# Kernel tuning notes

Measured on AMD Instinct MI355X. Metric: run time of the kernel, lower is better.

## Reference

```python
import jax, jax.numpy as jnp
import numpy as np

B, C = 4096, 10000
TAU = 1.0
MIN_K, MAX_K = 30, 100


def setup_inputs() -> dict:
    key = jax.random.key(0)
    k1, k2 = jax.random.split(key, 2)
    logit = jax.random.normal(k1, (B, C), dtype=jnp.float32)
    target = jax.random.randint(k2, (B,), 0, C)
    # long-tailed class counts: exponential decay from 1000 down to 5
    cls_num = np.exp(np.linspace(np.log(1000.0), np.log(5.0), C)).astype(np.float32)
    cls_num_ratio = cls_num / cls_num.sum()
    log_cls_num = jnp.asarray(np.log(cls_num_ratio + 1e-6), dtype=jnp.float32)
    freq = (cls_num.max() / cls_num).astype(np.float32)
    freq_norm = (freq - freq.min()) / (freq.max() - freq.min() + 1e-6)
    k_per_class = jnp.asarray((freq_norm * (MAX_K - MIN_K) + MIN_K).astype(np.int32))
    return {"logit": logit, "target": target, "log_cls_num": log_cls_num,
            "k_per_class": k_per_class}


def reference(logit, target, log_cls_num, k_per_class):
    b, c = logit.shape
    rows = jnp.arange(b)
    # logit-adjusted cross entropy (loss_full)
    logit_adj = logit + TAU * log_cls_num[None, :]
    log_p_adj = jax.nn.log_softmax(logit_adj, axis=1)  # [B, C]
    loss_full = -jnp.mean(log_p_adj[rows, target])
    # per-row variable-k top-k mask on the ORIGINAL logits
    prob_adj = jnp.exp(log_p_adj)
    k = jnp.minimum(k_per_class[target], c)            # [B]
    sorted_desc = -jnp.sort(-logit, axis=1)            # [B, C] descending
    thresh = sorted_desc[rows, k - 1]                  # k-th largest per row
    mask = logit >= thresh[:, None]
    masked_prob = jnp.where(mask, prob_adj, 0.0) + 1e-6
    masked_prob = masked_prob / masked_prob.sum(axis=1, keepdims=True)
    loss_topk = -jnp.mean(jnp.log(masked_prob)[rows, target])
    return 0.5 * loss_full + 0.5 * loss_topk
```

## Files before the change

kernel.cpp:

```cpp
#include <hip/hip_runtime.h>

#define BLOCK 256
#define C_DIM 10000
#define C4 (C_DIM / 4)
#define NIT ((C4 + BLOCK - 1) / BLOCK)
#define TAU 1.0f
#define CAP 2048
#define PIV_HI 2.0f
#define PIV_LO 1.0f

__device__ __forceinline__ unsigned flip_key(float f) {
    unsigned u = __float_as_uint(f);
    return (u & 0x80000000u) ? ~u : (u | 0x80000000u);
}
__device__ __forceinline__ float unflip_key(unsigned k) {
    unsigned u = (k & 0x80000000u) ? (k & 0x7fffffffu) : ~k;
    return __uint_as_float(u);
}

__global__ void zero_out_kernel(float* out, int n) {
    int i = blockIdx.x * blockDim.x + threadIdx.x;
    if (i < n) out[i] = 0.f;
}

__device__ __forceinline__ void scan_pick(unsigned* hist, int shift, int tid,
                                          unsigned* shp, unsigned* shkr, unsigned* shcnt) {
    unsigned h0 = hist[4 * tid + 0], h1 = hist[4 * tid + 1];
    unsigned h2 = hist[4 * tid + 2], h3 = hist[4 * tid + 3];
    unsigned loc = h0 + h1 + h2 + h3;
    unsigned suf = loc;
    for (int off = 1; off < 64; off <<= 1) {
        unsigned o = __shfl_down(suf, off);
        if (tid + off < 64) suf += o;
    }
    unsigned sufex = suf - loc;
    unsigned kr = *shkr;
    unsigned s3 = sufex + h3;
    unsigned s2 = s3 + h2;
    unsigned s1 = s2 + h1;
    unsigned s0 = s1 + h0;
    int bsel = -1; unsigned newkr = 0, newcnt = 0;
    if      (s3 >= kr && s3 - h3 < kr) { bsel = 4 * tid + 3; newkr = kr - (s3 - h3); newcnt = h3; }
    else if (s2 >= kr && s2 - h2 < kr) { bsel = 4 * tid + 2; newkr = kr - (s2 - h2); newcnt = h2; }
    else if (s1 >= kr && s1 - h1 < kr) { bsel = 4 * tid + 1; newkr = kr - (s1 - h1); newcnt = h1; }
    else if (s0 >= kr && s0 - h0 < kr) { bsel = 4 * tid + 0; newkr = kr - (s0 - h0); newcnt = h0; }
    if (bsel >= 0) {
        *shp |= ((unsigned)bsel << shift);
        *shkr = newkr;
        *shcnt = newcnt;
    }
}

__global__ __launch_bounds__(BLOCK, 8) void topk_la_loss_kernel(
    const float* __restrict__ logit, const int* __restrict__ target,
    const float* __restrict__ lcn, const int* __restrict__ kpc,
    float* __restrict__ out, int B) {
    __shared__ unsigned hist[256];
    __shared__ unsigned candk[CAP];
    __shared__ unsigned short candi[CAP];
    __shared__ float red_a[4], red_b[4];
    __shared__ unsigned sh_nc, sh_prefix, sh_kr, sh_cnt;
    __shared__ int sh_path, sh_k;
    __shared__ float sh_thresh, sh_madj;

    const int row = blockIdx.x;
    const int tid = threadIdx.x;
    const int lane = tid & 63;
    const int wid = tid >> 6;
    const float* lrow = logit + (size_t)row * C_DIM;

    if (tid == 0) {
        int t = target[row];
        int k = kpc[t];
        if (k > C_DIM) k = C_DIM;
        sh_k = k;
        sh_nc = 0u;
    }
    __syncthreads();

    float z = 0.f, madj = -INFINITY;
    for (int it = 0; it < NIT; ++it) {
        int j4 = it * BLOCK + tid;
        if (j4 < C4) {
            float4 f = ((const float4*)lrow)[j4];
            float4 l = ((const float4*)lcn)[j4];
            float a0 = f.x + TAU * l.x, a1 = f.y + TAU * l.y;
            float a2 = f.z + TAU * l.z, a3 = f.w + TAU * l.w;
            z += __expf(a0) + __expf(a1) + __expf(a2) + __expf(a3);
            madj = fmaxf(madj, fmaxf(fmaxf(a0, a1), fmaxf(a2, a3)));
            int j = 4 * j4;
            if (f.x >= PIV_HI) { unsigned i = atomicAdd(&sh_nc, 1u); if (i < CAP) { candk[i] = __float_as_uint(f.x); candi[i] = (unsigned short)(j + 0); } }
            if (f.y >= PIV_HI) { unsigned i = atomicAdd(&sh_nc, 1u); if (i < CAP) { candk[i] = __float_as_uint(f.y); candi[i] = (unsigned short)(j + 1); } }
            if (f.z >= PIV_HI) { unsigned i = atomicAdd(&sh_nc, 1u); if (i < CAP) { candk[i] = __float_as_uint(f.z); candi[i] = (unsigned short)(j + 2); } }
            if (f.w >= PIV_HI) { unsigned i = atomicAdd(&sh_nc, 1u); if (i < CAP) { candk[i] = __float_as_uint(f.w); candi[i] = (unsigned short)(j + 3); } }
        }
    }
    for (int off = 32; off; off >>= 1) madj = fmaxf(madj, __shfl_down(madj, off));
    if (lane == 0) red_a[wid] = madj;
    __syncthreads();

    if (tid == 0) {
        sh_madj = fmaxf(fmaxf(red_a[0], red_a[1]), fmaxf(red_a[2], red_a[3]));
        unsigned n = sh_nc;
        unsigned k = (unsigned)sh_k;
        sh_path = (n >= k && n <= CAP) ? 0 : ((n < k) ? 1 : 2);
        sh_kr = k;
        sh_prefix = 0u;
        sh_cnt = n;
    }
    __syncthreads();

    if (sh_path == 1) {
        if (tid == 0) sh_nc = 0u;
        __syncthreads();
        for (int it = 0; it < NIT; ++it) {
            int j4 = it * BLOCK + tid;
            if (j4 < C4) {
                float4 f = ((const float4*)lrow)[j4];
                int j = 4 * j4;
                if (f.x >= PIV_LO) { unsigned i = atomicAdd(&sh_nc, 1u); if (i < CAP) { candk[i] = __float_as_uint(f.x); candi[i] = (unsigned short)(j + 0); } }
                if (f.y >= PIV_LO) { unsigned i = atomicAdd(&sh_nc, 1u); if (i < CAP) { candk[i] = __float_as_uint(f.y); candi[i] = (unsigned short)(j + 1); } }
                if (f.z >= PIV_LO) { unsigned i = atomicAdd(&sh_nc, 1u); if (i < CAP) { candk[i] = __float_as_uint(f.z); candi[i] = (unsigned short)(j + 2); } }
                if (f.w >= PIV_LO) { unsigned i = atomicAdd(&sh_nc, 1u); if (i < CAP) { candk[i] = __float_as_uint(f.w); candi[i] = (unsigned short)(j + 3); } }
            }
        }
        __syncthreads();
        if (tid == 0) {
            unsigned n = sh_nc;
            unsigned k = (unsigned)sh_k;
            sh_path = (n >= k && n <= CAP) ? 0 : 2;
            sh_kr = k;
            sh_prefix = 0u;
            sh_cnt = n;
        }
        __syncthreads();
    }

    const int path = sh_path;
    const float madjB = sh_madj;

    if (path == 0) {
        const int nc = (int)sh_cnt;
        unsigned kmask = 0u;
        for (int q = 0; q < 4; ++q) {
            if (sh_cnt == 1u) break;
            const int shift = 24 - 8 * q;
            hist[tid] = 0u;
            __syncthreads();
            const unsigned pref = sh_prefix;
            for (int i = tid; i < nc; i += BLOCK) {
                unsigned kk = candk[i];
                if ((kk & kmask) == pref) atomicAdd(&hist[(kk >> shift) & 0xFFu], 1u);
            }
            __syncthreads();
            if (tid < 64) scan_pick(hist, shift, tid, &sh_prefix, &sh_kr, &sh_cnt);
            kmask |= (0xFFu << shift);
            __syncthreads();
        }
        if (sh_cnt == 1u && kmask != 0xFFFFFFFFu) {
            const unsigned pref = sh_prefix;
            __syncthreads();
            for (int i = tid; i < nc; i += BLOCK) {
                unsigned kk = candk[i];
                if ((kk & kmask) == pref) sh_prefix = kk;
            }
            __syncthreads();
        }
        if (tid == 0) sh_thresh = __uint_as_float(sh_prefix);
    } else {
        for (int p = 0; p < 4; ++p) {
            const int shift = 24 - 8 * p;
            const unsigned pmask = p ? (0xFFFFFFFFu << (shift + 8)) : 0u;
            hist[tid] = 0u;
            __syncthreads();
            const unsigned pref = sh_prefix;
            for (int it = 0; it < NIT; ++it) {
                int j4 = it * BLOCK + tid;
                if (j4 < C4) {
                    float4 f = ((const float4*)lrow)[j4];
                    unsigned kk;
                    kk = flip_key(f.x); if ((kk & pmask) == pref) atomicAdd(&hist[(kk >> shift) & 0xFFu], 1u);
                    kk = flip_key(f.y); if ((kk & pmask) == pref) atomicAdd(&hist[(kk >> shift) & 0xFFu], 1u);
                    kk = flip_key(f.z); if ((kk & pmask) == pref) atomicAdd(&hist[(kk >> shift) & 0xFFu], 1u);
                    kk = flip_key(f.w); if ((kk & pmask) == pref) atomicAdd(&hist[(kk >> shift) & 0xFFu], 1u);
                }
            }
            __syncthreads();
            if (tid < 64) scan_pick(hist, shift, tid, &sh_prefix, &sh_kr, &sh_cnt);
            __syncthreads();
        }
        if (tid == 0) sh_thresh = unflip_key(sh_prefix);
    }
    __syncthreads();

    const float thresh = sh_thresh;
    const bool rare = fabsf(madjB) > 80.f;

    float sm = 0.f;
    if (!rare) {
        if (path == 0) {
            const int nc = (int)((sh_nc <= CAP) ? sh_nc : CAP);
            for (int i = tid; i < nc; i += BLOCK) {
                unsigned kk = candk[i];
                float v = __uint_as_float(kk);
                if (v >= thresh) sm += __expf(v + TAU * lcn[candi[i]]);
            }
        } else {
            for (int it = 0; it < NIT; ++it) {
                int j4 = it * BLOCK + tid;
                if (j4 < C4) {
                    float4 f = ((const float4*)lrow)[j4];
                    float4 l = ((const float4*)lcn)[j4];
                    if (f.x >= thresh) sm += __expf(f.x + TAU * l.x);
                    if (f.y >= thresh) sm += __expf(f.y + TAU * l.y);
                    if (f.z >= thresh) sm += __expf(f.z + TAU * l.z);
                    if (f.w >= thresh) sm += __expf(f.w + TAU * l.w);
                }
            }
        }
    } else {
        z = 0.f;
        for (int it = 0; it < NIT; ++it) {
            int j4 = it * BLOCK + tid;
            if (j4 < C4) {
                float4 f = ((const float4*)lrow)[j4];
                float4 l = ((const float4*)lcn)[j4];
                float e;
                e = __expf(f.x + TAU * l.x - madjB); z += e; if (f.x >= thresh) sm += e;
                e = __expf(f.y + TAU * l.y - madjB); z += e; if (f.y >= thresh) sm += e;
                e = __expf(f.z + TAU * l.z - madjB); z += e; if (f.z >= thresh) sm += e;
                e = __expf(f.w + TAU * l.w - madjB); z += e; if (f.w >= thresh) sm += e;
            }
        }
    }

    for (int off = 32; off; off >>= 1) {
        z  += __shfl_down(z, off);
        sm += __shfl_down(sm, off);
    }
    if (lane == 0) { red_a[wid] = z; red_b[wid] = sm; }
    __syncthreads();

    if (tid == 0) {
        float Z = red_a[0] + red_a[1] + red_a[2] + red_a[3];
        float S = red_b[0] + red_b[1] + red_b[2] + red_b[3];
        int t = target[row];
        float logit_t = lrow[t];
        float adj_t = logit_t + TAU * lcn[t];
        float sub = rare ? madjB : 0.f;
        float lpt = adj_t - sub - __logf(Z);
        float p_num = ((logit_t >= thresh) ? __expf(lpt) : 0.f) + 1e-6f;
        float Smask = S / Z + (float)C_DIM * 1e-6f;
        float loss = 0.5f * (-lpt + __logf(Smask) - __logf(p_num));
        atomicAdd(out, loss / (float)B);
    }
}

extern "C" void kernel_launch(void* const* d_in, const int* in_sizes, int n_in,
                              void* d_out, int out_size, void* d_ws, size_t ws_size,
                              hipStream_t stream) {
    const float* logit  = (const float*)d_in[0];
    const int*   target = (const int*)d_in[1];
    const float* lcn    = (const float*)d_in[2];
    const int*   kpc    = (const int*)d_in[3];
    float* out = (float*)d_out;
    const int B = in_sizes[1];

    zero_out_kernel<<<1, 64, 0, stream>>>(out, out_size);
    topk_la_loss_kernel<<<B, BLOCK, 0, stream>>>(logit, target, lcn, kpc, out, B);
}
```

Baseline: 268.0 us.

## Split row pass into segmented streaming kernel and candidate-based select kernel

```diff
diff --git a/kernel.cpp b/kernel.cpp
--- a/kernel.cpp
+++ b/kernel.cpp
@@ -5,9 +5,11 @@
 #define C4 (C_DIM / 4)
 #define NIT ((C4 + BLOCK - 1) / BLOCK)
 #define TAU 1.0f
-#define CAP 2048
-#define PIV_HI 2.0f
-#define PIV_LO 1.0f
+#define PIV 2.0f
+#define SEG 4
+#define SEGLEN (C_DIM / SEG)
+#define SEGLEN4 (SEGLEN / 4)
+#define MAXCAP 2048
 
 __device__ __forceinline__ unsigned flip_key(float f) {
     unsigned u = __float_as_uint(f);
@@ -18,9 +20,73 @@
     return __uint_as_float(u);
 }
 
-__global__ void zero_out_kernel(float* out, int n) {
+__global__ void init_kernel(float* out, int out_n, float* z, unsigned* madj,
+                            unsigned* cnt, int B) {
     int i = blockIdx.x * blockDim.x + threadIdx.x;
-    if (i < n) out[i] = 0.f;
+    if (i < out_n) out[i] = 0.f;
+    if (i < B) { z[i] = 0.f; madj[i] = 0u; cnt[i] = 0u; }
+}
+
+__device__ __forceinline__ void append_cand(bool m, float v, int idx, int lane,
+                                            unsigned* g_cnt_row,
+                                            float* __restrict__ cv,
+                                            unsigned short* __restrict__ ci, int cap) {
+    unsigned long long mk = __ballot(m);
+    if (mk == 0ull) return;
+    int leader = (int)(__ffsll((unsigned long long)mk) - 1);
+    unsigned n = (unsigned)__popcll(mk);
+    unsigned base = 0u;
+    if (lane == leader) base = atomicAdd(g_cnt_row, n);
+    base = (unsigned)__shfl((int)base, leader);
+    if (m) {
+        unsigned pos = base + (unsigned)__popcll(mk & ((1ull << lane) - 1ull));
+        if (pos < (unsigned)cap) { cv[pos] = v; ci[pos] = (unsigned short)idx; }
+    }
+}
+
+__global__ __launch_bounds__(BLOCK) void stream_kernel(
+    const float* __restrict__ logit, const float* __restrict__ lcn,
+    float* __restrict__ g_z, unsigned* __restrict__ g_madj,
+    unsigned* __restrict__ g_cnt, float* __restrict__ candval,
+    unsigned short* __restrict__ candidx, int cap) {
+    __shared__ float red_z[4], red_m[4];
+    const int row = blockIdx.x / SEG;
+    const int seg = blockIdx.x % SEG;
+    const int tid = threadIdx.x;
+    const int lane = tid & 63;
+    const int wid = tid >> 6;
+
+    const float* lr = logit + (size_t)row * C_DIM + seg * SEGLEN;
+    const float* lc = lcn + seg * SEGLEN;
+    float* cv = candval + (size_t)row * cap;
+    unsigned short* ci = candidx + (size_t)row * cap;
+
+    float z = 0.f, madj = -INFINITY;
+    for (int j4 = tid; j4 < SEGLEN4; j4 += BLOCK) {
+        float4 f = ((const float4*)lr)[j4];
+        float4 l = ((const float4*)lc)[j4];
+        float a0 = f.x + TAU * l.x, a1 = f.y + TAU * l.y;
+        float a2 = f.z + TAU * l.z, a3 = f.w + TAU * l.w;
+        z += __expf(a0) + __expf(a1) + __expf(a2) + __expf(a3);
+        madj = fmaxf(madj, fmaxf(fmaxf(a0, a1), fmaxf(a2, a3)));
+        int j = seg * SEGLEN + 4 * j4;
+        append_cand(f.x >= PIV, f.x, j + 0, lane, &g_cnt[row], cv, ci, cap);
+        append_cand(f.y >= PIV, f.y, j + 1, lane, &g_cnt[row], cv, ci, cap);
+        append_cand(f.z >= PIV, f.z, j + 2, lane, &g_cnt[row], cv, ci, cap);
+        append_cand(f.w >= PIV, f.w, j + 3, lane, &g_cnt[row], cv, ci, cap);
+    }
+    for (int off = 32; off; off >>= 1) {
+        z += __shfl_down(z, off);
+        madj = fmaxf(madj, __shfl_down(madj, off));
+    }
+    if (lane == 0) { red_z[wid] = z; red_m[wid] = madj; }
+    __syncthreads();
+    if (tid == 0) {
+        float zb = red_z[0] + red_z[1] + red_z[2] + red_z[3];
+        float mb = fmaxf(fmaxf(red_m[0], red_m[1]), fmaxf(red_m[2], red_m[3]));
+        atomicAdd(&g_z[row], zb);
+        atomicMax(&g_madj[row], flip_key(mb));
+    }
 }
 
 __device__ __forceinline__ void scan_pick(unsigned* hist, int shift, int tid,
@@ -51,17 +117,18 @@
     }
 }
 
-__global__ __launch_bounds__(BLOCK, 8) void topk_la_loss_kernel(
+__global__ __launch_bounds__(BLOCK) void select_kernel(
     const float* __restrict__ logit, const int* __restrict__ target,
     const float* __restrict__ lcn, const int* __restrict__ kpc,
+    const float* __restrict__ g_z, const unsigned* __restrict__ g_madj,
+    const unsigned* __restrict__ g_cnt, const float* __restrict__ candval,
+    const unsigned short* __restrict__ candidx, int cap,
     float* __restrict__ out, int B) {
+    __shared__ unsigned candk[MAXCAP];
     __shared__ unsigned hist[256];
-    __shared__ unsigned candk[CAP];
-    __shared__ unsigned short candi[CAP];
     __shared__ float red_a[4], red_b[4];
-    __shared__ unsigned sh_nc, sh_prefix, sh_kr, sh_cnt;
-    __shared__ int sh_path, sh_k;
-    __shared__ float sh_thresh, sh_madj;
+    __shared__ unsigned sh_prefix, sh_kr, sh_cnt;
+    __shared__ float sh_thresh;
 
     const int row = blockIdx.x;
     const int tid = threadIdx.x;
@@ -69,78 +136,23 @@
     const int wid = tid >> 6;
     const float* lrow = logit + (size_t)row * C_DIM;
 
-    if (tid == 0) {
-        int t = target[row];
-        int k = kpc[t];
-        if (k > C_DIM) k = C_DIM;
-        sh_k = k;
-        sh_nc = 0u;
-    }
-    __syncthreads();
-
-    float z = 0.f, madj = -INFINITY;
-    for (int it = 0; it < NIT; ++it) {
-        int j4 = it * BLOCK + tid;
-        if (j4 < C4) {
-            float4 f = ((const float4*)lrow)[j4];
-            float4 l = ((const float4*)lcn)[j4];
-            float a0 = f.x + TAU * l.x, a1 = f.y + TAU * l.y;
-            float a2 = f.z + TAU * l.z, a3 = f.w + TAU * l.w;
-            z += __expf(a0) + __expf(a1) + __expf(a2) + __expf(a3);
-            madj = fmaxf(madj, fmaxf(fmaxf(a0, a1), fmaxf(a2, a3)));
-            int j = 4 * j4;
-            if (f.x >= PIV_HI) { unsigned i = atomicAdd(&sh_nc, 1u); if (i < CAP) { candk[i] = __float_as_uint(f.x); candi[i] = (unsigned short)(j + 0); } }
-            if (f.y >= PIV_HI) { unsigned i = atomicAdd(&sh_nc, 1u); if (i < CAP) { candk[i] = __float_as_uint(f.y); candi[i] = (unsigned short)(j + 1); } }
-            if (f.z >= PIV_HI) { unsigned i = atomicAdd(&sh_nc, 1u); if (i < CAP) { candk[i] = __float_as_uint(f.z); candi[i] = (unsigned short)(j + 2); } }
-            if (f.w >= PIV_HI) { unsigned i = atomicAdd(&sh_nc, 1u); if (i < CAP) { candk[i] = __float_as_uint(f.w); candi[i] = (unsigned short)(j + 3); } }
-        }
-    }
-    for (int off = 32; off; off >>= 1) madj = fmaxf(madj, __shfl_down(madj, off));
-    if (lane == 0) red_a[wid] = madj;
-    __syncthreads();
-
-    if (tid == 0) {
-        sh_madj = fmaxf(fmaxf(red_a[0], red_a[1]), fmaxf(red_a[2], red_a[3]));
-        unsigned n = sh_nc;
-        unsigned k = (unsigned)sh_k;
-        sh_path = (n >= k && n <= CAP) ? 0 : ((n < k) ? 1 : 2);
-        sh_kr = k;
-        sh_prefix = 0u;
-        sh_cnt = n;
-    }
-    __syncthreads();
-
-    if (sh_path == 1) {
-        if (tid == 0) sh_nc = 0u;
+    const int t = target[row];
+    int k = kpc[t]; if (k > C_DIM) k = C_DIM;
+    const unsigned nc = g_cnt[row];
+    const float madj = unflip_key(g_madj[row]);
+    const float Zws = g_z[row];
+    const bool rare = fabsf(madj) > 80.f;
+    const bool normal = (!rare) && (cap > 0) && (nc >= (unsigned)k) && (nc <= (unsigned)cap);
+
+    float sm = 0.f, zloc = 0.f;
+
+    if (normal) {
+        const float* cv = candval + (size_t)row * cap;
+        const unsigned short* ci = candidx + (size_t)row * cap;
+        for (int i = tid; i < (int)nc; i += BLOCK) candk[i] = __float_as_uint(cv[i]);
+        if (tid == 0) { sh_prefix = 0u; sh_kr = (unsigned)k; sh_cnt = nc; }
         __syncthreads();
-        for (int it = 0; it < NIT; ++it) {
-            int j4 = it * BLOCK + tid;
-            if (j4 < C4) {
-                float4 f = ((const float4*)lrow)[j4];
-                int j = 4 * j4;
-                if (f.x >= PIV_LO) { unsigned i = atomicAdd(&sh_nc, 1u); if (i < CAP) { candk[i] = __float_as_uint(f.x); candi[i] = (unsigned short)(j + 0); } }
-                if (f.y >= PIV_LO) { unsigned i = atomicAdd(&sh_nc, 1u); if (i < CAP) { candk[i] = __float_as_uint(f.y); candi[i] = (unsigned short)(j + 1); } }
-                if (f.z >= PIV_LO) { unsigned i = atomicAdd(&sh_nc, 1u); if (i < CAP) { candk[i] = __float_as_uint(f.z); candi[i] = (unsigned short)(j + 2); } }
-                if (f.w >= PIV_LO) { unsigned i = atomicAdd(&sh_nc, 1u); if (i < CAP) { candk[i] = __float_as_uint(f.w); candi[i] = (unsigned short)(j + 3); } }
-            }
-        }
-        __syncthreads();
-        if (tid == 0) {
-            unsigned n = sh_nc;
-            unsigned k = (unsigned)sh_k;
-            sh_path = (n >= k && n <= CAP) ? 0 : 2;
-            sh_kr = k;
-            sh_prefix = 0u;
-            sh_cnt = n;
-        }
-        __syncthreads();
-    }
-
-    const int path = sh_path;
-    const float madjB = sh_madj;
-
-    if (path == 0) {
-        const int nc = (int)sh_cnt;
+
         unsigned kmask = 0u;
         for (int q = 0; q < 4; ++q) {
             if (sh_cnt == 1u) break;
@@ -148,7 +160,7 @@
             hist[tid] = 0u;
             __syncthreads();
             const unsigned pref = sh_prefix;
-            for (int i = tid; i < nc; i += BLOCK) {
+            for (int i = tid; i < (int)nc; i += BLOCK) {
                 unsigned kk = candk[i];
                 if ((kk & kmask) == pref) atomicAdd(&hist[(kk >> shift) & 0xFFu], 1u);
             }
@@ -160,14 +172,22 @@
         if (sh_cnt == 1u && kmask != 0xFFFFFFFFu) {
             const unsigned pref = sh_prefix;
             __syncthreads();
-            for (int i = tid; i < nc; i += BLOCK) {
+            for (int i = tid; i < (int)nc; i += BLOCK) {
                 unsigned kk = candk[i];
                 if ((kk & kmask) == pref) sh_prefix = kk;
             }
             __syncthreads();
         }
         if (tid == 0) sh_thresh = __uint_as_float(sh_prefix);
+        __syncthreads();
+
+        const float thresh = sh_thresh;
+        for (int i = tid; i < (int)nc; i += BLOCK) {
+            float v = __uint_as_float(candk[i]);
+            if (v >= thresh) sm += __expf(v + TAU * lcn[ci[i]]);
+        }
     } else {
+        if (tid == 0) { sh_prefix = 0u; sh_kr = (unsigned)k; sh_cnt = (unsigned)C_DIM; }
         for (int p = 0; p < 4; ++p) {
             const int shift = 24 - 8 * p;
             const unsigned pmask = p ? (0xFFFFFFFFu << (shift + 8)) : 0u;
@@ -190,67 +210,41 @@
             __syncthreads();
         }
         if (tid == 0) sh_thresh = unflip_key(sh_prefix);
-    }
-    __syncthreads();
-
-    const float thresh = sh_thresh;
-    const bool rare = fabsf(madjB) > 80.f;
-
-    float sm = 0.f;
-    if (!rare) {
-        if (path == 0) {
-            const int nc = (int)((sh_nc <= CAP) ? sh_nc : CAP);
-            for (int i = tid; i < nc; i += BLOCK) {
-                unsigned kk = candk[i];
-                float v = __uint_as_float(kk);
-                if (v >= thresh) sm += __expf(v + TAU * lcn[candi[i]]);
-            }
-        } else {
-            for (int it = 0; it < NIT; ++it) {
-                int j4 = it * BLOCK + tid;
-                if (j4 < C4) {
-                    float4 f = ((const float4*)lrow)[j4];
-                    float4 l = ((const float4*)lcn)[j4];
-                    if (f.x >= thresh) sm += __expf(f.x + TAU * l.x);
-                    if (f.y >= thresh) sm += __expf(f.y + TAU * l.y);
-                    if (f.z >= thresh) sm += __expf(f.z + TAU * l.z);
-                    if (f.w >= thresh) sm += __expf(f.w + TAU * l.w);
-                }
-            }
-        }
-    } else {
-        z = 0.f;
+        __syncthreads();
+
+        const float thresh = sh_thresh;
+        const float sub = rare ? madj : 0.f;
         for (int it = 0; it < NIT; ++it) {
             int j4 = it * BLOCK + tid;
             if (j4 < C4) {
                 float4 f = ((const float4*)lrow)[j4];
                 float4 l = ((const float4*)lcn)[j4];
                 float e;
-                e = __expf(f.x + TAU * l.x - madjB); z += e; if (f.x >= thresh) sm += e;
-                e = __expf(f.y + TAU * l.y - madjB); z += e; if (f.y >= thresh) sm += e;
-                e = __expf(f.z + TAU * l.z - madjB); z += e; if (f.z >= thresh) sm += e;
-                e = __expf(f.w + TAU * l.w - madjB); z += e; if (f.w >= thresh) sm += e;
+                e = __expf(f.x + TAU * l.x - sub); zloc += e; if (f.x >= thresh) sm += e;
+                e = __expf(f.y + TAU * l.y - sub); zloc += e; if (f.y >= thresh) sm += e;
+                e = __expf(f.z + TAU * l.z - sub); zloc += e; if (f.z >= thresh) sm += e;
+                e = __expf(f.w + TAU * l.w - sub); zloc += e; if (f.w >= thresh) sm += e;
             }
         }
     }
 
     for (int off = 32; off; off >>= 1) {
-        z  += __shfl_down(z, off);
-        sm += __shfl_down(sm, off);
-    }
-    if (lane == 0) { red_a[wid] = z; red_b[wid] = sm; }
+        sm   += __shfl_down(sm, off);
+        zloc += __shfl_down(zloc, off);
+    }
+    if (lane == 0) { red_a[wid] = zloc; red_b[wid] = sm; }
     __syncthreads();
 
     if (tid == 0) {
-        float Z = red_a[0] + red_a[1] + red_a[2] + red_a[3];
-        float S = red_b[0] + red_b[1] + red_b[2] + red_b[3];
-        int t = target[row];
+        float S  = red_b[0] + red_b[1] + red_b[2] + red_b[3];
+        float Zu = normal ? Zws : (red_a[0] + red_a[1] + red_a[2] + red_a[3]);
+        float thresh = sh_thresh;
         float logit_t = lrow[t];
         float adj_t = logit_t + TAU * lcn[t];
-        float sub = rare ? madjB : 0.f;
-        float lpt = adj_t - sub - __logf(Z);
+        float sub = rare ? madj : 0.f;
+        float lpt = adj_t - sub - __logf(Zu);
         float p_num = ((logit_t >= thresh) ? __expf(lpt) : 0.f) + 1e-6f;
-        float Smask = S / Z + (float)C_DIM * 1e-6f;
+        float Smask = S / Zu + (float)C_DIM * 1e-6f;
         float loss = 0.5f * (-lpt + __logf(Smask) - __logf(p_num));
         atomicAdd(out, loss / (float)B);
     }
@@ -266,6 +260,24 @@
     float* out = (float*)d_out;
     const int B = in_sizes[1];
 
-    zero_out_kernel<<<1, 64, 0, stream>>>(out, out_size);
-    topk_la_loss_kernel<<<B, BLOCK, 0, stream>>>(logit, target, lcn, kpc, out, B);
-}
+    char* ws = (char*)d_ws;
+    float*    g_z    = (float*)ws;
+    unsigned* g_madj = (unsigned*)(ws + (size_t)B * 4);
+    unsigned* g_cnt  = (unsigned*)(ws + (size_t)B * 8);
+    size_t fixed = (size_t)B * 12;
+    int cap = 0;
+    if (ws_size > fixed) {
+        size_t c = (ws_size - fixed) / ((size_t)B * 6);
+        cap = (c > (size_t)MAXCAP) ? MAXCAP : (int)c;
+        if (cap < 4) cap = 0;
+    }
+    float* candval = (float*)(ws + fixed);
+    unsigned short* candidx = (unsigned short*)(ws + fixed + (size_t)B * (size_t)cap * 4);
+
+    int initn = (out_size > B) ? out_size : B;
+    init_kernel<<<(initn + 255) / 256, 256, 0, stream>>>(out, out_size, g_z, g_madj, g_cnt, B);
+    stream_kernel<<<B * SEG, BLOCK, 0, stream>>>(logit, lcn, g_z, g_madj, g_cnt,
+                                                 candval, candidx, cap);
+    select_kernel<<<B, BLOCK, 0, stream>>>(logit, target, lcn, kpc, g_z, g_madj, g_cnt,
+                                           candval, candidx, cap, out, B);
+}
```

Result: slower. 421.0 us (+57.1%).
